# Performance work log

Hardware: AMD Instinct MI355X
Metric: run time of the kernel (lower is better)

The kernel has to match this reference:

```python
import jax, jax.numpy as jnp
import numpy as np


def setup_inputs() -> dict:
    key = jax.random.key(0)
    k1, k2 = jax.random.split(key)
    x = jax.random.normal(k1, (16, 2048, 512), dtype=jnp.float32)
    embed = jax.random.normal(k2, (4096, 512), dtype=jnp.float32)
    return {"x": x, "embed": embed}


def reference(x, embed):
    # encode: flatten leading dims, compute -||x - e||^2 via expansion, argmax
    shape = x.shape
    xf = x.reshape(-1, shape[-1])                       # [N, d]
    x_sq = jnp.sum(xf * xf, axis=1, keepdims=True)      # [N, 1]
    e_sq = jnp.sum(embed * embed, axis=1)[None, :]      # [1, K]
    dist = -(x_sq - 2.0 * (xf @ embed.T) + e_sq)        # [N, K]
    embed_ind = jnp.argmax(dist, axis=-1)               # [N]
    embed_ind = embed_ind.reshape(shape[:-1])           # [B, S]
    # decode: embedding lookup (dequantize)
    quantize = embed[embed_ind]                         # [B, S, d]
    return embed_ind, quantize
```

## Files before the change

### kernel.cpp

```cpp
#include <hip/hip_runtime.h>
#include <hip/hip_fp16.h>
#include <stdint.h>


typedef _Float16 f16;
typedef __attribute__((ext_vector_type(4))) _Float16 f16x4;
typedef __attribute__((ext_vector_type(8))) _Float16 f16x8;
typedef __attribute__((ext_vector_type(4))) float f32x4;

#define DDIM 512
#define KCODES 4096
#define NSPLIT 2
#define BM 256
#define BN 256
#define BK 32
#define NCH ((KCODES / NSPLIT) / BN)
#define NSTEPS (NCH * (DDIM / BK))
#define PSTRIDE (NSPLIT * 2)

__device__ __forceinline__ void gload_lds16(const void* g, void* l) {
  __builtin_amdgcn_global_load_lds(
      (const __attribute__((address_space(1))) void*)g,
      (__attribute__((address_space(3))) void*)l,
      16, 0, 0);
}

__global__ void convert_split(const float* __restrict__ in,
                              f16* __restrict__ hi, f16* __restrict__ lo, int n4) {
  int stride = gridDim.x * blockDim.x;
  for (int i = blockIdx.x * blockDim.x + threadIdx.x; i < n4; i += stride) {
    float4 v = ((const float4*)in)[i];
    float vv[4] = {v.x, v.y, v.z, v.w};
    f16x4 h, l;
#pragma unroll
    for (int j = 0; j < 4; ++j) {
      _Float16 hh = (_Float16)vv[j];
      h[j] = hh;
      l[j] = (_Float16)(vv[j] - (float)hh);
    }
    ((f16x4*)hi)[i] = h;
    ((f16x4*)lo)[i] = l;
  }
}

__global__ void esq_kernel(const float* __restrict__ e, float* __restrict__ esq) {
  int gw = (blockIdx.x * blockDim.x + threadIdx.x) >> 6;
  int lane = threadIdx.x & 63;
  if (gw >= KCODES) return;
  const float4* row = (const float4*)(e + (size_t)gw * DDIM);
  float4 a = row[lane * 2];
  float4 b = row[lane * 2 + 1];
  double s = (double)a.x * a.x + (double)a.y * a.y + (double)a.z * a.z + (double)a.w * a.w +
             (double)b.x * b.x + (double)b.y * b.y + (double)b.z * b.z + (double)b.w * b.w;
#pragma unroll
  for (int m = 32; m; m >>= 1) s += __shfl_xor(s, m, 64);
  if (lane == 0) esq[gw] = (float)s;
}

__global__ __launch_bounds__(512, 2) void vq_main(
    const f16* __restrict__ Ah, const f16* __restrict__ Al,
    const f16* __restrict__ Bh, const f16* __restrict__ Bl,
    const float* __restrict__ esq, float2* __restrict__ partials, int nRowBlocks) {
  __shared__ char lds[131072];

  int nwg = gridDim.x;
  int bid = blockIdx.x;
  int cpx = nwg >> 3;
  int swz = (bid & 7) * cpx + (bid >> 3);
  int nsp = swz / nRowBlocks;
  int brow = swz % nRowBlocks;
  int rowbase = brow * BM;

  int tid = threadIdx.x;
  int lane = tid & 63;
  int wv = tid >> 6;
  int wr = wv >> 1, wc = wv & 1;
  int l15 = lane & 15, lg = lane >> 4;

  const int aoff = (wr * 64 + l15) * 64 + lg * 16;
  const int boff = (wc * 128 + l15) * 64 + lg * 16;

  int srow = tid >> 2;
  int skoff = (tid & 3) * 8;
  const int codesPer = KCODES / NSPLIT;

  const f16* aSrcH = Ah + (size_t)(rowbase + srow) * DDIM + skoff;
  const f16* aSrcL = Al + (size_t)(rowbase + srow) * DDIM + skoff;
  const f16* bBaseH = Bh + (size_t)(nsp * codesPer + srow) * DDIM + skoff;
  const f16* bBaseL = Bl + (size_t)(nsp * codesPer + srow) * DDIM + skoff;

  auto STAGE = [&](int buf, int ch, int kk) {
    char* base = lds + buf * 65536 + wv * 1024;
    size_t bo = (size_t)(ch * BN) * DDIM + kk;
    gload_lds16(aSrcH + kk, base);
    gload_lds16(aSrcH + kk + (size_t)128 * DDIM, base + 8192);
    gload_lds16(aSrcL + kk, base + 16384);
    gload_lds16(aSrcL + kk + (size_t)128 * DDIM, base + 16384 + 8192);
    gload_lds16(bBaseH + bo, base + 32768);
    gload_lds16(bBaseH + bo + (size_t)128 * DDIM, base + 32768 + 8192);
    gload_lds16(bBaseL + bo, base + 49152);
    gload_lds16(bBaseL + bo + (size_t)128 * DDIM, base + 49152 + 8192);
  };

  float bestv[16];
  int besti[16];
#pragma unroll
  for (int t = 0; t < 16; ++t) { bestv[t] = -3.4e38f; besti[t] = 0; }

  f32x4 acc[4][8];

  STAGE(0, 0, 0);
  __syncthreads();

  int buf = 0;
#pragma unroll 1
  for (int s = 0; s < NSTEPS; ++s) {
    int ch = s >> 4;
    int ns = s + 1;
    if (ns < NSTEPS) STAGE(buf ^ 1, ns >> 4, (ns & 15) * BK);

    if ((s & 15) == 0) {
#pragma unroll
      for (int i = 0; i < 4; ++i)
#pragma unroll
        for (int j = 0; j < 8; ++j) acc[i][j] = (f32x4){0.f, 0.f, 0.f, 0.f};
    }

    char* base = lds + buf * 65536;
    f16x8 ah[4], al[4], bh[8], bl[8];
#pragma unroll
    for (int i = 0; i < 4; ++i) ah[i] = *(const f16x8*)(base + aoff + i * 1024);
#pragma unroll
    for (int j = 0; j < 8; ++j) bh[j] = *(const f16x8*)(base + 32768 + boff + j * 1024);
#pragma unroll
    for (int i = 0; i < 4; ++i)
#pragma unroll
      for (int j = 0; j < 8; ++j)
        acc[i][j] = __builtin_amdgcn_mfma_f32_16x16x32_f16(ah[i], bh[j], acc[i][j], 0, 0, 0);
#pragma unroll
    for (int i = 0; i < 4; ++i) al[i] = *(const f16x8*)(base + 16384 + aoff + i * 1024);
#pragma unroll
    for (int i = 0; i < 4; ++i)
#pragma unroll
      for (int j = 0; j < 8; ++j)
        acc[i][j] = __builtin_amdgcn_mfma_f32_16x16x32_f16(al[i], bh[j], acc[i][j], 0, 0, 0);
#pragma unroll
    for (int j = 0; j < 8; ++j) bl[j] = *(const f16x8*)(base + 49152 + boff + j * 1024);
#pragma unroll
    for (int i = 0; i < 4; ++i)
#pragma unroll
      for (int j = 0; j < 8; ++j)
        acc[i][j] = __builtin_amdgcn_mfma_f32_16x16x32_f16(ah[i], bl[j], acc[i][j], 0, 0, 0);

    if ((s & 15) == 15) {
      int cbase = nsp * codesPer + ch * BN;
#pragma unroll
      for (int j = 0; j < 8; ++j) {
        int code = cbase + wc * 128 + j * 16 + l15;
        float eh = 0.5f * esq[code];
#pragma unroll
        for (int i = 0; i < 4; ++i)
#pragma unroll
          for (int r = 0; r < 4; ++r) {
            float v = acc[i][j][r] - eh;
            int t = i * 4 + r;
            if (v > bestv[t]) { bestv[t] = v; besti[t] = code; }
          }
      }
    }
    __syncthreads();
    buf ^= 1;
  }

#pragma unroll
  for (int m = 1; m < 16; m <<= 1) {
#pragma unroll
    for (int t = 0; t < 16; ++t) {
      float ov = __shfl_xor(bestv[t], m, 64);
      int oi = __shfl_xor(besti[t], m, 64);
      if (ov > bestv[t] || (ov == bestv[t] && oi < besti[t])) { bestv[t] = ov; besti[t] = oi; }
    }
  }
  if (l15 == 0) {
#pragma unroll
    for (int i = 0; i < 4; ++i)
#pragma unroll
      for (int r = 0; r < 4; ++r) {
        int row = rowbase + wr * 64 + i * 16 + lg * 4 + r;
        partials[(size_t)row * PSTRIDE + nsp * 2 + wc] =
            make_float2(bestv[i * 4 + r], (float)besti[i * 4 + r]);
      }
  }
}

__global__ void reduce_decode(const float* __restrict__ embed,
                              const float2* __restrict__ partials,
                              float* __restrict__ outIdx, float* __restrict__ outQ,
                              int nRows) {
  int gw = (blockIdx.x * blockDim.x + threadIdx.x) >> 6;
  int lane = threadIdx.x & 63;
  if (gw >= nRows) return;
  float bv = -3.4e38f;
  int bi = 0x7fffffff;
#pragma unroll
  for (int s = 0; s < PSTRIDE; ++s) {
    float2 p = partials[(size_t)gw * PSTRIDE + s];
    int idx = (int)p.y;
    if (p.x > bv || (p.x == bv && idx < bi)) { bv = p.x; bi = idx; }
  }
  if (lane == 0) outIdx[gw] = (float)bi;
  const float4* src = (const float4*)(embed + (size_t)bi * DDIM);
  float4* dst = (float4*)(outQ + (size_t)gw * DDIM);
  dst[lane] = src[lane];
  dst[lane + 64] = src[lane + 64];
}

extern "C" void kernel_launch(void* const* d_in, const int* in_sizes, int n_in,
                              void* d_out, int out_size, void* d_ws, size_t ws_size,
                              hipStream_t stream) {
  const float* x = (const float*)d_in[0];
  const float* embed = (const float*)d_in[1];
  int nX = in_sizes[0];
  int nRows = nX / DDIM;
  int nRowBlocks = nRows / BM;

  float* out = (float*)d_out;
  float* outIdx = out;
  float* outQ = out + nRows;

  size_t szA = (size_t)nRows * DDIM * sizeof(f16);
  size_t szB = (size_t)KCODES * DDIM * sizeof(f16);
  size_t szEsq = (size_t)KCODES * sizeof(float);
  size_t szPart = (size_t)nRows * PSTRIDE * sizeof(float2);

  char* ws = (char*)d_ws;
  f16 *Ah, *Al, *Bh, *Bl;
  float* esq;
  float2* parts;
  size_t needFull = 2 * szA + 2 * szB + szEsq + szPart;
  if (ws_size >= needFull) {
    Ah = (f16*)ws;
    Al = (f16*)(ws + szA);
    Bh = (f16*)(ws + 2 * szA);
    Bl = (f16*)(ws + 2 * szA + szB);
    esq = (float*)(ws + 2 * szA + 2 * szB);
    parts = (float2*)(ws + 2 * szA + 2 * szB + szEsq);
  } else {
    Ah = (f16*)outQ;
    Al = Ah + (size_t)nRows * DDIM;
    Bh = (f16*)ws;
    Bl = (f16*)(ws + szB);
    esq = (float*)(ws + 2 * szB);
    parts = (float2*)(ws + 2 * szB + szEsq);
  }

  int n4x = nX / 4;
  int n4e = in_sizes[1] / 4;
  hipLaunchKernelGGL(convert_split, dim3(2048), dim3(256), 0, stream, x, Ah, Al, n4x);
  hipLaunchKernelGGL(convert_split, dim3((n4e + 255) / 256), dim3(256), 0, stream, embed, Bh, Bl, n4e);
  hipLaunchKernelGGL(esq_kernel, dim3(KCODES / 4), dim3(256), 0, stream, embed, esq);
  hipLaunchKernelGGL(vq_main, dim3(nRowBlocks * NSPLIT), dim3(512), 0, stream,
                     Ah, Al, Bh, Bl, esq, parts, nRowBlocks);
  hipLaunchKernelGGL(reduce_decode, dim3(nRows / 4), dim3(256), 0, stream,
                     embed, parts, outIdx, outQ, nRows);
}
```

Baseline: 379.4 us.

## Use partial vmcnt waits, split barriers, setprio around MFMA, and LDS-cached esq

Replaces the end-of-step __syncthreads with an explicit s_waitcnt vmcnt(8) plus s_barrier at the top of each step, so the next stage's global→LDS loads stay in flight while the current buffer is consumed. MFMA blocks are wrapped in s_setprio to favour matrix issue across co-resident waves. The halved code norms are preloaded once into LDS instead of being read from global memory in each epilogue. Correctness depends on the hand-counted vmcnt matching the eight loads issued per stage and on the compiler not reordering around the sched barriers.

```diff
diff --git a/kernel.cpp b/kernel.cpp
--- a/kernel.cpp
+++ b/kernel.cpp
@@ -62,6 +62,7 @@
     const f16* __restrict__ Bh, const f16* __restrict__ Bl,
     const float* __restrict__ esq, float2* __restrict__ partials, int nRowBlocks) {
   __shared__ char lds[131072];
+  __shared__ float esqLds[KCODES / NSPLIT];
 
   int nwg = gridDim.x;
   int bid = blockIdx.x;
@@ -109,15 +110,26 @@
 
   f32x4 acc[4][8];
 
+  {
+    float4 ev = ((const float4*)(esq + nsp * codesPer))[tid];
+    ((float4*)esqLds)[tid] = make_float4(0.5f * ev.x, 0.5f * ev.y, 0.5f * ev.z, 0.5f * ev.w);
+  }
   STAGE(0, 0, 0);
   __syncthreads();
 
-  int buf = 0;
 #pragma unroll 1
   for (int s = 0; s < NSTEPS; ++s) {
+    int cur = s & 1;
     int ch = s >> 4;
     int ns = s + 1;
-    if (ns < NSTEPS) STAGE(buf ^ 1, ns >> 4, (ns & 15) * BK);
+    if (ns < NSTEPS) {
+      STAGE(cur ^ 1, ns >> 4, (ns & 15) * BK);
+      asm volatile("s_waitcnt vmcnt(8)" ::: "memory");
+    } else {
+      asm volatile("s_waitcnt vmcnt(0)" ::: "memory");
+    }
+    __builtin_amdgcn_s_barrier();
+    __builtin_amdgcn_sched_barrier(0);
 
     if ((s & 15) == 0) {
 #pragma unroll
@@ -126,38 +138,44 @@
         for (int j = 0; j < 8; ++j) acc[i][j] = (f32x4){0.f, 0.f, 0.f, 0.f};
     }
 
-    char* base = lds + buf * 65536;
+    char* base = lds + cur * 65536;
     f16x8 ah[4], al[4], bh[8], bl[8];
 #pragma unroll
     for (int i = 0; i < 4; ++i) ah[i] = *(const f16x8*)(base + aoff + i * 1024);
 #pragma unroll
     for (int j = 0; j < 8; ++j) bh[j] = *(const f16x8*)(base + 32768 + boff + j * 1024);
+    __builtin_amdgcn_s_setprio(1);
 #pragma unroll
     for (int i = 0; i < 4; ++i)
 #pragma unroll
       for (int j = 0; j < 8; ++j)
         acc[i][j] = __builtin_amdgcn_mfma_f32_16x16x32_f16(ah[i], bh[j], acc[i][j], 0, 0, 0);
+    __builtin_amdgcn_s_setprio(0);
 #pragma unroll
     for (int i = 0; i < 4; ++i) al[i] = *(const f16x8*)(base + 16384 + aoff + i * 1024);
+    __builtin_amdgcn_s_setprio(1);
 #pragma unroll
     for (int i = 0; i < 4; ++i)
 #pragma unroll
       for (int j = 0; j < 8; ++j)
         acc[i][j] = __builtin_amdgcn_mfma_f32_16x16x32_f16(al[i], bh[j], acc[i][j], 0, 0, 0);
+    __builtin_amdgcn_s_setprio(0);
 #pragma unroll
     for (int j = 0; j < 8; ++j) bl[j] = *(const f16x8*)(base + 49152 + boff + j * 1024);
+    __builtin_amdgcn_s_setprio(1);
 #pragma unroll
     for (int i = 0; i < 4; ++i)
 #pragma unroll
       for (int j = 0; j < 8; ++j)
         acc[i][j] = __builtin_amdgcn_mfma_f32_16x16x32_f16(ah[i], bl[j], acc[i][j], 0, 0, 0);
+    __builtin_amdgcn_s_setprio(0);
 
     if ((s & 15) == 15) {
-      int cbase = nsp * codesPer + ch * BN;
+      int cloc = ch * BN + wc * 128;
 #pragma unroll
       for (int j = 0; j < 8; ++j) {
-        int code = cbase + wc * 128 + j * 16 + l15;
-        float eh = 0.5f * esq[code];
+        float eh = esqLds[cloc + j * 16 + l15];
+        int code = nsp * codesPer + cloc + j * 16 + l15;
 #pragma unroll
         for (int i = 0; i < 4; ++i)
 #pragma unroll
@@ -168,8 +186,8 @@
           }
       }
     }
-    __syncthreads();
-    buf ^= 1;
+    __builtin_amdgcn_sched_barrier(0);
+    __builtin_amdgcn_s_barrier();
   }
 
 #pragma unroll
```

After: 410.8 us. 8.3% more time.
